# Kernel optimization log

Measured on AMD Instinct MI355X. Metric: run time of the kernel, lower is better.

The kernel has to match this reference:

```python
import jax, jax.numpy as jnp
import numpy as np

RES, IN, OUT = 1024, 16, 8
LEAK = 0.7
SPECTRAL_RADIUS = 0.9
CONNECTIVITY = 0.1


def _init_reservoir(rng):
    W = rng.standard_normal((RES, RES)).astype(np.float32)
    mask = rng.random((RES, RES)) > CONNECTIVITY
    W[mask] = 0.0
    sr = np.max(np.abs(np.linalg.eigvals(W)))
    return (W * (SPECTRAL_RADIUS / sr)).astype(np.float32)


def setup_inputs() -> dict:
    key = jax.random.key(0)
    k1, k2, k3, k4 = jax.random.split(key, 4)
    rng = np.random.default_rng(0)
    B, S = 32, 4096
    x = jax.random.normal(k1, (B, S, IN), dtype=jnp.float32)
    state = jnp.zeros((B, RES), dtype=jnp.float32)
    W_in = jax.random.normal(k2, (RES, IN), dtype=jnp.float32)
    W_res = jnp.asarray(_init_reservoir(rng))
    lim = 1.0 / np.sqrt(RES)
    W_out_w = jax.random.uniform(k3, (OUT, RES), minval=-lim, maxval=lim, dtype=jnp.float32)
    W_out_b = jax.random.uniform(k4, (OUT,), minval=-lim, maxval=lim, dtype=jnp.float32)
    return {"x": x, "state": state, "W_in": W_in, "W_res": W_res,
            "W_out_w": W_out_w, "W_out_b": W_out_b}


def reference(x, state, W_in, W_res, W_out_w, W_out_b):
    # Precompute input projections for all steps: [B, S, RES]
    inp = jnp.einsum('bsi,ri->bsr', x, W_in)

    def step(h, u_t):
        # u_t: [B, RES] precomputed input term at time t
        new_h = (1.0 - LEAK) * h + LEAK * jnp.tanh(u_t + h @ W_res.T)
        return new_h, new_h

    # scan over time axis
    final_state, states = jax.lax.scan(step, state, jnp.swapaxes(inp, 0, 1))
    states = jnp.swapaxes(states, 0, 1)  # [B, S, RES]
    outputs = jnp.einsum('bsr,or->bso', states, W_out_w) + W_out_b
    return outputs, final_state
```

## Files before the change

### kernel.cpp

```cpp
#include <hip/hip_runtime.h>
#include <stdint.h>

#define RES     1024
#define INPD    16
#define OUTD    8
#define BATCH   32
#define SEQ     4096
#define NCMAX   24
#define PASSPAD 3

#define MAT_BYTES ((size_t)NCMAX * RES * 8 * 4)

__global__ __launch_bounds__(32) void esn_count(const float* __restrict__ W,
                                                uint32_t* __restrict__ eff) {
  const int r = blockIdx.x, b = threadIdx.x;
  const float* row = W + (size_t)r * RES;
  int n = 0;
  for (int k = 0; k < 32; ++k) n += (row[b + 32 * k] != 0.0f) ? 1 : 0;
  int t3 = (n > PASSPAD) ? (n - PASSPAD) : 0;
  for (int o = 16; o; o >>= 1) t3 += __shfl_down(t3, o, 32);
  if (b == 0) eff[r] = (uint32_t)(PASSPAD * 32 + t3);
}

__global__ __launch_bounds__(1024) void esn_sort(const uint32_t* __restrict__ eff,
                                                 uint32_t* __restrict__ perm,
                                                 uint32_t* __restrict__ wnc) {
  __shared__ uint32_t key[RES];
  const int tid = threadIdx.x;
  key[tid] = (eff[tid] << 10) | (uint32_t)tid;
  __syncthreads();
  for (int len = 2; len <= RES; len <<= 1) {
    for (int s = len >> 1; s > 0; s >>= 1) {
      const int j = tid ^ s;
      if (j > tid) {
        const uint32_t a = key[tid], c = key[j];
        const bool up = ((tid & len) == 0);
        if ((a > c) == up) { key[tid] = c; key[j] = a; }
      }
      __syncthreads();
    }
  }
  const uint32_t k = key[tid];
  perm[tid] = k & 1023u;
  if ((tid & 63) == 63) {
    uint32_t c = ((k >> 10) + 7u) >> 3;
    wnc[tid >> 6] = (c < (uint32_t)NCMAX) ? c : (uint32_t)NCMAX;
  }
}

__global__ __launch_bounds__(32) void esn_pack(const float* __restrict__ W,
                                               const uint32_t* __restrict__ perm,
                                               uint32_t* __restrict__ mato) {
  const int p = blockIdx.x;
  const int b = threadIdx.x;
  __shared__ float    vls[32][16];
  __shared__ uint16_t cls[32][16];
  __shared__ int      cnt[32];
  __shared__ uint32_t rr;
  if (b == 0) rr = perm[p];
  __syncthreads();
  const float* row = W + (size_t)rr * RES;

  int n = 0;
  for (int k = 0; k < 32; ++k) {
    const float v = row[b + 32 * k];
    if (v != 0.0f && n < 16) { vls[b][n] = v; cls[b][n] = (uint16_t)(b + 32 * k); ++n; }
  }
  cnt[b] = n;
  const int rot = p & 31;
  for (int e = b; e < NCMAX * 8; e += 32) {
    const uint32_t padcol = (uint32_t)((rot + (e & 31)) & 31);
    mato[(size_t)(e >> 3) * (RES * 8) + (size_t)p * 8 + (e & 7)] = padcol << 18;
  }
  __syncthreads();

  const int myord = (b - rot) & 31;
  for (int k2 = 0; k2 < n; ++k2) {
    int rank;
    if (k2 < PASSPAD) {
      rank = k2 * 32 + myord;
    } else {
      rank = PASSPAD * 32;
      const int kp = k2 - PASSPAD;
      for (int b2 = 0; b2 < 32; ++b2) {
        int cp = cnt[b2] - PASSPAD; cp = (cp > 0) ? cp : 0;
        const int ord = (b2 - rot) & 31;
        const int lim = kp + ((ord < myord) ? 1 : 0);
        rank += (cp < lim) ? cp : lim;
      }
    }
    if (rank < NCMAX * 8) {
      const uint32_t u  = __float_as_uint(vls[b][k2]);
      const uint32_t bf = (u + 0x7FFFu + ((u >> 16) & 1u)) >> 16;
      mato[(size_t)(rank >> 3) * (RES * 8) + (size_t)p * 8 + (rank & 7)] =
          ((uint32_t)cls[b][k2] << 18) | bf;
    }
  }
}

#define GATHER8(QA, QB)                                                       \
  a0 = fmaf(__uint_as_float((QA).x << 16), hc[(QA).x >> 18], a0);             \
  a1 = fmaf(__uint_as_float((QA).y << 16), hc[(QA).y >> 18], a1);             \
  a2 = fmaf(__uint_as_float((QA).z << 16), hc[(QA).z >> 18], a2);             \
  a3 = fmaf(__uint_as_float((QA).w << 16), hc[(QA).w >> 18], a3);             \
  a0 = fmaf(__uint_as_float((QB).x << 16), hc[(QB).x >> 18], a0);             \
  a1 = fmaf(__uint_as_float((QB).y << 16), hc[(QB).y >> 18], a1);             \
  a2 = fmaf(__uint_as_float((QB).z << 16), hc[(QB).z >> 18], a2);             \
  a3 = fmaf(__uint_as_float((QB).w << 16), hc[(QB).w >> 18], a3);

__global__ __launch_bounds__(1024) void esn_scan(
    const float* __restrict__ x, const float* __restrict__ state,
    const float* __restrict__ Win, const float* __restrict__ Woutw,
    const float* __restrict__ Woutb,
    const uint32_t* __restrict__ mat, const uint32_t* __restrict__ perm,
    const uint32_t* __restrict__ wnc,
    float* __restrict__ out) {
  __shared__ float  hbuf[2][RES];
  __shared__ float4 xbuf[2][INPD / 4];

  const int b    = blockIdx.x;
  const int tid  = threadIdx.x;
  const int wave = tid >> 6;
  const int lane = tid & 63;
  const int row  = (int)perm[tid];
  const int ncw  = (int)__builtin_amdgcn_readfirstlane(wnc[wave]);

  const float4* winp = (const float4*)(Win + (size_t)row * INPD);
  const float4 w0 = winp[0], w1 = winp[1], w2 = winp[2], w3 = winp[3];

  float wo[16];
  const float* wor = Woutw + (size_t)wave * RES;
#pragma unroll
  for (int j = 0; j < 16; ++j) wo[j] = (wave < OUTD) ? wor[lane + 64 * j] : 0.0f;
  const float bw = (wave < OUTD) ? Woutb[wave] : 0.0f;

  float hreg = state[(size_t)b * RES + row];
  hbuf[0][row] = hreg;
  const float* xr = x + (size_t)b * SEQ * INPD;
  if (tid < INPD / 4) xbuf[0][tid] = ((const float4*)xr)[tid];
  __syncthreads();

  const uint32_t* mp = mat + (size_t)tid * 8;
  float* finals = out + (size_t)BATCH * SEQ * OUTD;

  for (int t = 0; t < SEQ; ++t) {
    const int par = t & 1;
    const float* hc = hbuf[par];

    if (t > 0 && wave < OUTD) {
      float s = 0.0f;
#pragma unroll
      for (int j = 0; j < 16; ++j) s = fmaf(hc[lane + 64 * j], wo[j], s);
#pragma unroll
      for (int d = 1; d < 64; d <<= 1) s += __shfl_xor(s, d);
      if (lane == 0) out[((size_t)b * SEQ + (t - 1)) * OUTD + wave] = s + bw;
    }
    if (tid < INPD / 4 && t + 1 < SEQ)
      xbuf[par ^ 1][tid] = ((const float4*)(xr + (size_t)(t + 1) * INPD))[tid];

    const float4 xa = xbuf[par][0], xbv = xbuf[par][1];
    const float4 xc = xbuf[par][2], xd  = xbuf[par][3];
    float a0 = 0.f, a1 = 0.f, a2 = 0.f, a3 = 0.f;
    a0 = fmaf(xa.x, w0.x, a0);  a1 = fmaf(xa.y, w0.y, a1);
    a2 = fmaf(xa.z, w0.z, a2);  a3 = fmaf(xa.w, w0.w, a3);
    a0 = fmaf(xbv.x, w1.x, a0); a1 = fmaf(xbv.y, w1.y, a1);
    a2 = fmaf(xbv.z, w1.z, a2); a3 = fmaf(xbv.w, w1.w, a3);
    a0 = fmaf(xc.x, w2.x, a0);  a1 = fmaf(xc.y, w2.y, a1);
    a2 = fmaf(xc.z, w2.z, a2);  a3 = fmaf(xc.w, w2.w, a3);
    a0 = fmaf(xd.x, w3.x, a0);  a1 = fmaf(xd.y, w3.y, a1);
    a2 = fmaf(xd.z, w3.z, a2);  a3 = fmaf(xd.w, w3.w, a3);

    uint4 qa = *(const uint4*)mp;
    uint4 qb = *(const uint4*)(mp + 4);
    for (int c = 0; c < ncw - 1; ++c) {
      const uint32_t* cpn = mp + (size_t)(c + 1) * (RES * 8);
      const uint4 na = *(const uint4*)cpn;
      const uint4 nb = *(const uint4*)(cpn + 4);
      GATHER8(qa, qb)
      qa = na; qb = nb;
    }
    GATHER8(qa, qb)

    const float acc = (a0 + a1) + (a2 + a3);
    const float e   = exp2f(acc * 2.885390081777927f);
    const float th  = 1.0f - 2.0f * __builtin_amdgcn_rcpf(e + 1.0f);
    const float hn  = fmaf(0.7f, th, 0.3f * hreg);
    hreg = hn;
    hbuf[par ^ 1][row] = hn;
    __syncthreads();
  }

  if (wave < OUTD) {
    float s = 0.0f;
#pragma unroll
    for (int j = 0; j < 16; ++j) s = fmaf(hbuf[0][lane + 64 * j], wo[j], s);
#pragma unroll
    for (int d = 1; d < 64; d <<= 1) s += __shfl_xor(s, d);
    if (lane == 0) out[((size_t)b * SEQ + (SEQ - 1)) * OUTD + wave] = s + bw;
  }
  finals[(size_t)b * RES + row] = hreg;
}

extern "C" void kernel_launch(void* const* d_in, const int* in_sizes, int n_in,
                              void* d_out, int out_size, void* d_ws, size_t ws_size,
                              hipStream_t stream) {
  const float* x     = (const float*)d_in[0];
  const float* state = (const float*)d_in[1];
  const float* Win   = (const float*)d_in[2];
  const float* Wres  = (const float*)d_in[3];
  const float* Woutw = (const float*)d_in[4];
  const float* Woutb = (const float*)d_in[5];
  float* out = (float*)d_out;

  uint8_t*  ws   = (uint8_t*)d_ws;
  uint32_t* mat  = (uint32_t*)ws;
  uint32_t* eff  = (uint32_t*)(ws + MAT_BYTES);
  uint32_t* perm = (uint32_t*)(ws + MAT_BYTES + 4096);
  uint32_t* wnc  = (uint32_t*)(ws + MAT_BYTES + 8192);

  esn_count<<<RES, 32, 0, stream>>>(Wres, eff);
  esn_sort<<<1, RES, 0, stream>>>(eff, perm, wnc);
  esn_pack<<<RES, 32, 0, stream>>>(Wres, perm, mat);
  esn_scan<<<BATCH, RES, 0, stream>>>(x, state, Win, Woutw, Woutb,
                                      mat, perm, wnc, out);
}
```

Baseline: 19.07 ms.

## Split each batch's recurrence across four cooperating blocks with global-memory exchange

Each batch element's scan is now spread over four workgroups, each owning a quarter of the reservoir rows. Within a block the sparse matrix chunks are split into four segments held in registers, and partial sums are reduced through shared memory. After every time step each block publishes its new hidden-state slice to global memory, signals a counter and spins on its peers' counters before pulling their slices back into shared memory. The aim is to raise CU utilisation and remove the per-step sparse-matrix reloads, at the cost of a cross-block barrier and a global-memory round trip every step, plus the risk of deadlock if all 128 blocks are not resident at once.

Measured after the change: 20.30 ms. 6.4% more time.

```diff
diff --git a/kernel.cpp b/kernel.cpp
--- a/kernel.cpp
+++ b/kernel.cpp
@@ -8,6 +8,9 @@
 #define SEQ     4096
 #define NCMAX   24
 #define PASSPAD 3
+#define GROUP   4
+#define NBLK    (BATCH * GROUP)
+#define KMAX    6
 
 #define MAT_BYTES ((size_t)NCMAX * RES * 8 * 4)
 
@@ -98,6 +101,10 @@
   }
 }
 
+__global__ void esn_init(uint32_t* __restrict__ cnt) {
+  if (threadIdx.x < NBLK) cnt[threadIdx.x] = 0;
+}
+
 #define GATHER8(QA, QB)                                                       \
   a0 = fmaf(__uint_as_float((QA).x << 16), hc[(QA).x >> 18], a0);             \
   a1 = fmaf(__uint_as_float((QA).y << 16), hc[(QA).y >> 18], a1);             \
@@ -114,91 +121,130 @@
     const float* __restrict__ Woutb,
     const uint32_t* __restrict__ mat, const uint32_t* __restrict__ perm,
     const uint32_t* __restrict__ wnc,
+    uint32_t* __restrict__ cnt, float* __restrict__ pub,
     float* __restrict__ out) {
-  __shared__ float  hbuf[2][RES];
+  __shared__ float hbuf[2][RES];
   __shared__ float4 xbuf[2][INPD / 4];
-
-  const int b    = blockIdx.x;
+  __shared__ __align__(16) float psum[256][4];
+  __shared__ uint32_t perml[RES];
+
+  const int bid  = blockIdx.x;
+  const int grp  = bid >> 2;
+  const int role = bid & 3;
   const int tid  = threadIdx.x;
-  const int wave = tid >> 6;
-  const int lane = tid & 63;
-  const int row  = (int)perm[tid];
-  const int ncw  = (int)__builtin_amdgcn_readfirstlane(wnc[wave]);
-
-  const float4* winp = (const float4*)(Win + (size_t)row * INPD);
-  const float4 w0 = winp[0], w1 = winp[1], w2 = winp[2], w3 = winp[3];
+  const int l    = tid & 63;
+  const int v    = tid >> 6;
+  const int seg  = v >> 2;
+  const int lw   = v & 3;
+  const int W    = lw * 4 + role;
+  const int p    = W * 64 + l;
+  const int row  = (int)perm[p];
+  const int ncw  = ((int)__builtin_amdgcn_readfirstlane(wnc[W]) + 3 - seg) >> 2;
+
+  perml[tid] = perm[tid];
+
+  const float4 w4 = ((const float4*)(Win + (size_t)row * INPD))[seg];
 
   float wo[16];
-  const float* wor = Woutw + (size_t)wave * RES;
-#pragma unroll
-  for (int j = 0; j < 16; ++j) wo[j] = (wave < OUTD) ? wor[lane + 64 * j] : 0.0f;
-  const float bw = (wave < OUTD) ? Woutb[wave] : 0.0f;
-
-  float hreg = state[(size_t)b * RES + row];
-  hbuf[0][row] = hreg;
-  const float* xr = x + (size_t)b * SEQ * INPD;
+  const float* wor = Woutw + (size_t)v * RES;
+#pragma unroll
+  for (int j = 0; j < 16; ++j) wo[j] = (v < OUTD) ? wor[l + 64 * j] : 0.0f;
+  const float bw = (v < OUTD) ? Woutb[v] : 0.0f;
+
+  uint4 qa[KMAX], qb[KMAX];
+#pragma unroll
+  for (int k = 0; k < KMAX; ++k) {
+    if (k < ncw) {
+      const uint32_t* cp = mat + (size_t)(seg + 4 * k) * (RES * 8) + (size_t)p * 8;
+      qa[k] = *(const uint4*)cp;
+      qb[k] = *(const uint4*)(cp + 4);
+    } else {
+      qa[k] = make_uint4(0, 0, 0, 0);
+      qb[k] = make_uint4(0, 0, 0, 0);
+    }
+  }
+
+  hbuf[0][tid] = state[(size_t)grp * RES + tid];
+  float hreg = (tid < 256) ? state[(size_t)grp * RES + row] : 0.0f;
+  const float* xr = x + (size_t)grp * SEQ * INPD;
   if (tid < INPD / 4) xbuf[0][tid] = ((const float4*)xr)[tid];
   __syncthreads();
-
-  const uint32_t* mp = mat + (size_t)tid * 8;
-  float* finals = out + (size_t)BATCH * SEQ * OUTD;
 
   for (int t = 0; t < SEQ; ++t) {
     const int par = t & 1;
     const float* hc = hbuf[par];
 
-    if (t > 0 && wave < OUTD) {
+    if (t > 0 && role == ((t - 1) & 3) && v < OUTD) {
       float s = 0.0f;
 #pragma unroll
-      for (int j = 0; j < 16; ++j) s = fmaf(hc[lane + 64 * j], wo[j], s);
+      for (int j = 0; j < 16; ++j) s = fmaf(hc[l + 64 * j], wo[j], s);
 #pragma unroll
       for (int d = 1; d < 64; d <<= 1) s += __shfl_xor(s, d);
-      if (lane == 0) out[((size_t)b * SEQ + (t - 1)) * OUTD + wave] = s + bw;
-    }
-    if (tid < INPD / 4 && t + 1 < SEQ)
-      xbuf[par ^ 1][tid] = ((const float4*)(xr + (size_t)(t + 1) * INPD))[tid];
-
-    const float4 xa = xbuf[par][0], xbv = xbuf[par][1];
-    const float4 xc = xbuf[par][2], xd  = xbuf[par][3];
+      if (l == 0) out[((size_t)grp * SEQ + (t - 1)) * OUTD + v] = s + bw;
+    }
+    if (v == 15 && l < INPD / 4 && t + 1 < SEQ)
+      xbuf[par ^ 1][l] = ((const float4*)(xr + (size_t)(t + 1) * INPD))[l];
+
+    const float4 xv = xbuf[par][seg];
     float a0 = 0.f, a1 = 0.f, a2 = 0.f, a3 = 0.f;
-    a0 = fmaf(xa.x, w0.x, a0);  a1 = fmaf(xa.y, w0.y, a1);
-    a2 = fmaf(xa.z, w0.z, a2);  a3 = fmaf(xa.w, w0.w, a3);
-    a0 = fmaf(xbv.x, w1.x, a0); a1 = fmaf(xbv.y, w1.y, a1);
-    a2 = fmaf(xbv.z, w1.z, a2); a3 = fmaf(xbv.w, w1.w, a3);
-    a0 = fmaf(xc.x, w2.x, a0);  a1 = fmaf(xc.y, w2.y, a1);
-    a2 = fmaf(xc.z, w2.z, a2);  a3 = fmaf(xc.w, w2.w, a3);
-    a0 = fmaf(xd.x, w3.x, a0);  a1 = fmaf(xd.y, w3.y, a1);
-    a2 = fmaf(xd.z, w3.z, a2);  a3 = fmaf(xd.w, w3.w, a3);
-
-    uint4 qa = *(const uint4*)mp;
-    uint4 qb = *(const uint4*)(mp + 4);
-    for (int c = 0; c < ncw - 1; ++c) {
-      const uint32_t* cpn = mp + (size_t)(c + 1) * (RES * 8);
-      const uint4 na = *(const uint4*)cpn;
-      const uint4 nb = *(const uint4*)(cpn + 4);
-      GATHER8(qa, qb)
-      qa = na; qb = nb;
-    }
-    GATHER8(qa, qb)
-
-    const float acc = (a0 + a1) + (a2 + a3);
-    const float e   = exp2f(acc * 2.885390081777927f);
-    const float th  = 1.0f - 2.0f * __builtin_amdgcn_rcpf(e + 1.0f);
-    const float hn  = fmaf(0.7f, th, 0.3f * hreg);
-    hreg = hn;
-    hbuf[par ^ 1][row] = hn;
-    __syncthreads();
-  }
-
-  if (wave < OUTD) {
-    float s = 0.0f;
-#pragma unroll
-    for (int j = 0; j < 16; ++j) s = fmaf(hbuf[0][lane + 64 * j], wo[j], s);
-#pragma unroll
-    for (int d = 1; d < 64; d <<= 1) s += __shfl_xor(s, d);
-    if (lane == 0) out[((size_t)b * SEQ + (SEQ - 1)) * OUTD + wave] = s + bw;
-  }
-  finals[(size_t)b * RES + row] = hreg;
+    a0 = fmaf(xv.x, w4.x, a0); a1 = fmaf(xv.y, w4.y, a1);
+    a2 = fmaf(xv.z, w4.z, a2); a3 = fmaf(xv.w, w4.w, a3);
+#pragma unroll
+    for (int k = 0; k < KMAX; ++k) {
+      if (k < ncw) { GATHER8(qa[k], qb[k]) }
+    }
+    psum[lw * 64 + l][seg] = (a0 + a1) + (a2 + a3);
+    __syncthreads();
+
+    float* ppub = pub + ((size_t)(par ^ 1) * BATCH + grp) * RES;
+    if (tid < 256) {
+      const float4 ps = *(const float4*)&psum[tid][0];
+      const float acc = (ps.x + ps.y) + (ps.z + ps.w);
+      const float e  = exp2f(acc * 2.885390081777927f);
+      const float th = 1.0f - 2.0f * __builtin_amdgcn_rcpf(e + 1.0f);
+      const float hn = fmaf(0.7f, th, 0.3f * hreg);
+      hreg = hn;
+      hbuf[par ^ 1][row] = hn;
+      __hip_atomic_store(&ppub[p], hn, __ATOMIC_RELAXED,
+                         __HIP_MEMORY_SCOPE_AGENT);
+    }
+    __syncthreads();
+
+    if (tid == 0)
+      __hip_atomic_store(&cnt[bid], (uint32_t)(t + 1), __ATOMIC_RELEASE,
+                         __HIP_MEMORY_SCOPE_AGENT);
+    if (tid < GROUP && tid != role) {
+      const uint32_t want = (uint32_t)(t + 1);
+      while (__hip_atomic_load(&cnt[grp * GROUP + tid], __ATOMIC_ACQUIRE,
+                               __HIP_MEMORY_SCOPE_AGENT) < want)
+        __builtin_amdgcn_s_sleep(2);
+    }
+    __syncthreads();
+
+    if (v >= 4) {
+      const int j  = v - 4;
+      const int gg = j / 3, m = j - gg * 3;
+      const int ro = m + ((m >= role) ? 1 : 0);
+      const int pp = (gg * 4 + ro) * 64 + l;
+      const float hv = __hip_atomic_load(&ppub[pp], __ATOMIC_RELAXED,
+                                         __HIP_MEMORY_SCOPE_AGENT);
+      hbuf[par ^ 1][perml[pp]] = hv;
+    }
+    __syncthreads();
+  }
+
+  if (role == 0) {
+    if (v < OUTD) {
+      float s = 0.0f;
+#pragma unroll
+      for (int j = 0; j < 16; ++j) s = fmaf(hbuf[0][l + 64 * j], wo[j], s);
+#pragma unroll
+      for (int d = 1; d < 64; d <<= 1) s += __shfl_xor(s, d);
+      if (l == 0) out[((size_t)grp * SEQ + (SEQ - 1)) * OUTD + v] = s + bw;
+    }
+    float* finals = out + (size_t)BATCH * SEQ * OUTD;
+    finals[(size_t)grp * RES + tid] = hbuf[0][tid];
+  }
 }
 
 extern "C" void kernel_launch(void* const* d_in, const int* in_sizes, int n_in,
@@ -217,10 +263,13 @@
   uint32_t* eff  = (uint32_t*)(ws + MAT_BYTES);
   uint32_t* perm = (uint32_t*)(ws + MAT_BYTES + 4096);
   uint32_t* wnc  = (uint32_t*)(ws + MAT_BYTES + 8192);
+  uint32_t* cnt  = (uint32_t*)(ws + MAT_BYTES + 12288);
+  float*    pub  = (float*)(ws + MAT_BYTES + 16384);
 
   esn_count<<<RES, 32, 0, stream>>>(Wres, eff);
   esn_sort<<<1, RES, 0, stream>>>(eff, perm, wnc);
   esn_pack<<<RES, 32, 0, stream>>>(Wres, perm, mat);
-  esn_scan<<<BATCH, RES, 0, stream>>>(x, state, Win, Woutw, Woutb,
-                                      mat, perm, wnc, out);
-}
+  esn_init<<<1, 128, 0, stream>>>(cnt);
+  esn_scan<<<NBLK, RES, 0, stream>>>(x, state, Win, Woutw, Woutb,
+                                     mat, perm, wnc, cnt, pub, out);
+}
```

## Replace rotation packing with greedy bank-conflict-aware gather scheduler

Applied to the files above, without the earlier changes.

Replaces the rotation-based sparse packing with a per-wave greedy scheduler, run once before the recurrence. In each gather slot it lets at most two lanes of a 64-lane wave hit the same LDS bank, so the h-vector gathers in the scan loop should be free of bank conflicts. Each wave's chunk count now comes from the schedule itself rather than from sorted nonzero counts. In exchange, the scheduler can emit extra padding slots, and entries beyond the per-bank depth or overflow caps are silently dropped.

Result: slower. 25.55 ms (+33.9%).

```diff
diff --git a/kernel.cpp b/kernel.cpp
--- a/kernel.cpp
+++ b/kernel.cpp
@@ -7,7 +7,8 @@
 #define BATCH   32
 #define SEQ     4096
 #define NCMAX   24
-#define PASSPAD 3
+#define DEPTH   13
+#define OVMAX   6
 
 #define MAT_BYTES ((size_t)NCMAX * RES * 8 * 4)
 
@@ -17,14 +18,12 @@
   const float* row = W + (size_t)r * RES;
   int n = 0;
   for (int k = 0; k < 32; ++k) n += (row[b + 32 * k] != 0.0f) ? 1 : 0;
-  int t3 = (n > PASSPAD) ? (n - PASSPAD) : 0;
-  for (int o = 16; o; o >>= 1) t3 += __shfl_down(t3, o, 32);
-  if (b == 0) eff[r] = (uint32_t)(PASSPAD * 32 + t3);
+  for (int o = 16; o; o >>= 1) n += __shfl_down(n, o, 32);
+  if (b == 0) eff[r] = (uint32_t)n;
 }
 
 __global__ __launch_bounds__(1024) void esn_sort(const uint32_t* __restrict__ eff,
-                                                 uint32_t* __restrict__ perm,
-                                                 uint32_t* __restrict__ wnc) {
+                                                 uint32_t* __restrict__ perm) {
   __shared__ uint32_t key[RES];
   const int tid = threadIdx.x;
   key[tid] = (eff[tid] << 10) | (uint32_t)tid;
@@ -40,60 +39,121 @@
       __syncthreads();
     }
   }
-  const uint32_t k = key[tid];
-  perm[tid] = k & 1023u;
-  if ((tid & 63) == 63) {
-    uint32_t c = ((k >> 10) + 7u) >> 3;
-    wnc[tid >> 6] = (c < (uint32_t)NCMAX) ? c : (uint32_t)NCMAX;
-  }
-}
-
-__global__ __launch_bounds__(32) void esn_pack(const float* __restrict__ W,
-                                               const uint32_t* __restrict__ perm,
-                                               uint32_t* __restrict__ mato) {
-  const int p = blockIdx.x;
-  const int b = threadIdx.x;
-  __shared__ float    vls[32][16];
-  __shared__ uint16_t cls[32][16];
-  __shared__ int      cnt[32];
-  __shared__ uint32_t rr;
-  if (b == 0) rr = perm[p];
-  __syncthreads();
-  const float* row = W + (size_t)rr * RES;
-
-  int n = 0;
-  for (int k = 0; k < 32; ++k) {
-    const float v = row[b + 32 * k];
-    if (v != 0.0f && n < 16) { vls[b][n] = v; cls[b][n] = (uint16_t)(b + 32 * k); ++n; }
-  }
-  cnt[b] = n;
-  const int rot = p & 31;
-  for (int e = b; e < NCMAX * 8; e += 32) {
-    const uint32_t padcol = (uint32_t)((rot + (e & 31)) & 31);
-    mato[(size_t)(e >> 3) * (RES * 8) + (size_t)p * 8 + (e & 7)] = padcol << 18;
-  }
-  __syncthreads();
-
-  const int myord = (b - rot) & 31;
-  for (int k2 = 0; k2 < n; ++k2) {
-    int rank;
-    if (k2 < PASSPAD) {
-      rank = k2 * 32 + myord;
+  perm[tid] = key[tid] & 1023u;
+}
+
+__global__ __launch_bounds__(64) void esn_sched(const float* __restrict__ W,
+                                                const uint32_t* __restrict__ perm,
+                                                uint32_t* __restrict__ mato,
+                                                uint32_t* __restrict__ wnc) {
+  __shared__ uint16_t cols[64][32][DEPTH];
+  __shared__ uint32_t cnt[64][32];
+  __shared__ uint32_t bankctr[32];
+  __shared__ uint16_t ovf[64][OVMAX];
+  __shared__ uint32_t ovn[64];
+  const int wv = blockIdx.x;
+  const int l  = threadIdx.x;
+  const int p  = wv * 64 + l;
+  const int row = (int)perm[p];
+
+  for (int i = l; i < 64 * 32; i += 64) ((uint32_t*)cnt)[i] = 0;
+  ovn[l] = 0;
+  __syncthreads();
+
+  for (int r2 = 0; r2 < 64; ++r2) {
+    const float* wr = W + (size_t)perm[wv * 64 + r2] * RES;
+    for (int k = 0; k < 16; ++k) {
+      const int c = k * 64 + l;
+      const float v = wr[c];
+      if (v != 0.0f) {
+        const int b = c & 31;
+        const uint32_t d = atomicAdd(&cnt[r2][b], 1u);
+        if (d < DEPTH) cols[r2][b][d] = (uint16_t)c;
+        else { const uint32_t o = atomicAdd(&ovn[r2], 1u);
+               if (o < OVMAX) ovf[r2][o] = (uint16_t)c; }
+      }
+    }
+  }
+  __syncthreads();
+
+  int trem = 0;
+  for (int b = 0; b < 32; ++b) {
+    uint32_t c = cnt[l][b];
+    if (c > DEPTH) { cnt[l][b] = DEPTH; c = DEPTH; }
+    trem += (int)c;
+  }
+  int myov = (int)ovn[l]; if (myov > OVMAX) myov = OVMAX;
+  trem += myov;
+
+  int wns = NCMAX * 8;
+  for (int s = 0; s < NCMAX * 8; ++s) {
+    if (l < 32) bankctr[l] = 0;
+    __syncthreads();
+
+    int emit = -1;
+    if (trem > 0) {
+      uint32_t tried = 0;
+      for (int it = 0; it < 6 && emit < 0; ++it) {
+        int bb = -1; uint32_t bc = 0;
+        for (int b = 0; b < 32; ++b) {
+          if (tried & (1u << b)) continue;
+          const uint32_t c = cnt[l][b];
+          if (c > bc) { bc = c; bb = b; }
+        }
+        if (bb < 0) break;
+        const uint32_t old = atomicAdd(&bankctr[bb], 1u);
+        if (old < 2u) {
+          const uint32_t d = cnt[l][bb] - 1u;
+          cnt[l][bb] = d;
+          emit = (int)cols[l][bb][d];
+          --trem;
+        } else { atomicSub(&bankctr[bb], 1u); tried |= 1u << bb; }
+      }
+      if (emit < 0 && myov > 0) {
+        const int c = (int)ovf[l][myov - 1];
+        const int b = c & 31;
+        if (!(tried & (1u << b))) {
+          const uint32_t old = atomicAdd(&bankctr[b], 1u);
+          if (old < 2u) { emit = c; --myov; --trem; }
+          else atomicSub(&bankctr[b], 1u);
+        }
+      }
+    }
+
+    uint32_t word;
+    if (emit >= 0) {
+      word = ((uint32_t)emit << 18) | 0x10000u;
     } else {
-      rank = PASSPAD * 32;
-      const int kp = k2 - PASSPAD;
-      for (int b2 = 0; b2 < 32; ++b2) {
-        int cp = cnt[b2] - PASSPAD; cp = (cp > 0) ? cp : 0;
-        const int ord = (b2 - rot) & 31;
-        const int lim = kp + ((ord < myord) ? 1 : 0);
-        rank += (cp < lim) ? cp : lim;
-      }
-    }
-    if (rank < NCMAX * 8) {
-      const uint32_t u  = __float_as_uint(vls[b][k2]);
-      const uint32_t bf = (u + 0x7FFFu + ((u >> 16) & 1u)) >> 16;
-      mato[(size_t)(rank >> 3) * (RES * 8) + (size_t)p * 8 + (rank & 7)] =
-          ((uint32_t)cls[b][k2] << 18) | bf;
+      int pb = -1;
+      for (int i = 0; i < 32; ++i) {
+        const int b = (l + s + i) & 31;
+        const uint32_t old = atomicAdd(&bankctr[b], 1u);
+        if (old < 2u) { pb = b; break; }
+        atomicSub(&bankctr[b], 1u);
+      }
+      if (pb < 0) pb = l & 31;
+      word = (uint32_t)pb << 18;
+    }
+    mato[(size_t)(s >> 3) * (RES * 8) + (size_t)p * 8 + (s & 7)] = word;
+
+    if (__ballot(trem > 0) == 0ull) { wns = s + 1; break; }
+    __syncthreads();
+  }
+
+  const int wfin = (wns + 7) & ~7;
+  for (int s = wns; s < wfin; ++s)
+    mato[(size_t)(s >> 3) * (RES * 8) + (size_t)p * 8 + (s & 7)] =
+        ((uint32_t)((l + s) & 31)) << 18;
+  if (l == 0) wnc[wv] = (uint32_t)(wfin >> 3);
+
+  const float* wr = W + (size_t)row * RES;
+  for (int s = 0; s < wns; ++s) {
+    const size_t off = (size_t)(s >> 3) * (RES * 8) + (size_t)p * 8 + (s & 7);
+    const uint32_t u = mato[off];
+    if (u & 0x10000u) {
+      const uint32_t fu = __float_as_uint(wr[u >> 18]);
+      const uint32_t bf = (fu + 0x7FFFu + ((fu >> 16) & 1u)) >> 16;
+      mato[off] = (u & 0xFFFC0000u) | bf;
     }
   }
 }
@@ -219,8 +279,8 @@
   uint32_t* wnc  = (uint32_t*)(ws + MAT_BYTES + 8192);
 
   esn_count<<<RES, 32, 0, stream>>>(Wres, eff);
-  esn_sort<<<1, RES, 0, stream>>>(eff, perm, wnc);
-  esn_pack<<<RES, 32, 0, stream>>>(Wres, perm, mat);
+  esn_sort<<<1, RES, 0, stream>>>(eff, perm);
+  esn_sched<<<16, 64, 0, stream>>>(Wres, perm, mat, wnc);
   esn_scan<<<BATCH, RES, 0, stream>>>(x, state, Win, Woutw, Woutb,
                                       mat, perm, wnc, out);
 }
```
